# Kernel tuning notes

Measured on AMD Instinct MI355X. Metric: run time of the kernel, lower is better.

The kernel has to match this reference:

```python
import jax, jax.numpy as jnp
import numpy as np

EPS = 1.1920929e-07  # torch RMSNorm default eps = float32 finfo eps

def rms_norm(x, w):
    return x * jax.lax.rsqrt(jnp.mean(x * x, axis=-1, keepdims=True) + EPS) * w

def setup_inputs() -> dict:
    key = jax.random.key(0)
    ks = jax.random.split(key, 10)
    B, C, H, W = 8, 64, 48, 48
    E = C  # embed_dim = query_dim = key_dim = value_dim
    q = jax.random.normal(ks[0], (B, C, H, W), jnp.float32)
    k = jax.random.normal(ks[1], (B, C, H, W), jnp.float32)
    v = jax.random.normal(ks[2], (B, C, H, W), jnp.float32)
    s = 1.0 / np.sqrt(E)
    conv_w = jax.random.normal(ks[3], (C, C, 3, 3), jnp.float32) * (1.0 / np.sqrt(C * 9))
    nq_w = jnp.ones((E,), jnp.float32)
    nk_w = jnp.ones((E,), jnp.float32)
    wq = jax.random.normal(ks[4], (E, E), jnp.float32) * s
    bq = jax.random.normal(ks[5], (E,), jnp.float32) * 0.01
    wk = jax.random.normal(ks[6], (E, E), jnp.float32) * s
    bk = jax.random.normal(ks[7], (E,), jnp.float32) * 0.01
    return {"q": q, "k": k, "v": v, "conv_w": conv_w, "nq_w": nq_w,
            "nk_w": nk_w, "wq": wq, "bq": bq, "wk": wk, "bk": bk}

def reference(q, k, v, conv_w, nq_w, nk_w, wq, bq, wk, bk):
    B, C, H, W = q.shape
    num_heads = 4
    head_dim = C // num_heads
    # conv2d 3x3, stride 1, same padding, no bias
    qc = jax.lax.conv_general_dilated(
        q, conv_w, window_strides=(1, 1), padding='SAME',
        dimension_numbers=('NCHW', 'OIHW', 'NCHW'))
    # b c h w -> b (h w) c
    qs = qc.reshape(B, C, H * W).transpose(0, 2, 1)
    ksq = k.reshape(B, C, -1).transpose(0, 2, 1)
    vsq = v.reshape(B, C, -1).transpose(0, 2, 1)
    # RMSNorm on q and k (norm_v output feeds MHA value path whose output is discarded)
    qn = rms_norm(qs, nq_w)
    kn = rms_norm(ksq, nk_w)
    # MHA projections (q scaled by 1/sqrt(head_dim) as in torch)
    qp = (qn @ wq.T + bq) * (1.0 / np.sqrt(head_dim))
    kp = ksq_p = kn @ wk.T + bk
    Sq, Sk = qp.shape[1], kp.shape[1]
    qh = qp.reshape(B, Sq, num_heads, head_dim)
    kh = kp.reshape(B, Sk, num_heads, head_dim)
    scores = jnp.einsum('bihd,bjhd->bhij', qh, kh)
    attn = jax.nn.softmax(scores, axis=-1)
    # average_attn_weights=True -> mean over heads
    attn_avg = jnp.mean(attn, axis=1)  # [b, i, j]
    # custom output: weighted sum over RAW (un-normed, unprojected) value
    out = jnp.einsum('bij,bjd->bid', attn_avg, vsq)
    return out
```

## Files before the change

kernel.cpp:

```cpp
#include <hip/hip_runtime.h>
#include <hip/hip_bf16.h>

namespace {
constexpr int kB = 8;
constexpr int kC = 64;
constexpr int kH = 48;
constexpr int kW = 48;
constexpr int kS = kH * kW;
constexpr float kEps = 1.1920929e-07f;
constexpr float kQScale = 0.25f * 1.4426950408889634f;
}

typedef __attribute__((ext_vector_type(8))) short short8;
typedef __attribute__((ext_vector_type(4))) float f32x4;

__device__ __forceinline__ short f2bf(float x) {
  unsigned u = __float_as_uint(x);
  u += 0x7fffu + ((u >> 16) & 1u);
  return (short)(u >> 16);
}
__device__ __forceinline__ float bf2f(short s) {
  return __uint_as_float(((unsigned)(unsigned short)s) << 16);
}
__device__ __forceinline__ float fexp2(float x) {
  return __builtin_amdgcn_exp2f(x);
}

__global__ __launch_bounds__(256) void prep_lite(
    const float* __restrict__ v, const float* __restrict__ wq,
    const float* __restrict__ wk, const float* __restrict__ conv_w,
    short* __restrict__ vq, short* __restrict__ wqb3, short* __restrict__ wkb3,
    short* __restrict__ wt3, float* __restrict__ out) {
  const int blk = blockIdx.x;
  const int t = threadIdx.x;
  if (blk < 576) {
    int g = blk * 256 + t;
    int bb = g / 18432;
    int rem = g - bb * 18432;
    int jseg = rem >> 8;
    int sub = rem & 255;
    int d = sub >> 6;
    int Lq = sub & 63;
    const float* src = v + ((size_t)(bb * 64 + d * 16 + (Lq & 15))) * kS
                         + jseg * 32 + (Lq >> 4) * 8;
    float4 x0 = *reinterpret_cast<const float4*>(src);
    float4 x1 = *reinterpret_cast<const float4*>(src + 4);
    short8 o;
    o[0] = f2bf(x0.x); o[1] = f2bf(x0.y); o[2] = f2bf(x0.z); o[3] = f2bf(x0.w);
    o[4] = f2bf(x1.x); o[5] = f2bf(x1.y); o[6] = f2bf(x1.z); o[7] = f2bf(x1.w);
    *reinterpret_cast<short8*>(vq + (size_t)g * 8) = o;
  } else if (blk < 752) {
    int idx = (blk - 576) * 256 + t;
    if (idx < 4096) {
      int j = idx & 7, Lw = (idx >> 3) & 63, slab = idx >> 9;
      int nt = slab & 3, kh = slab >> 2;
      int e = nt * 16 + (Lw & 15), c = kh * 32 + (Lw >> 4) * 8 + j;
      wqb3[idx] = f2bf(wq[e * 64 + c]);
    } else if (idx < 8192) {
      int i2 = idx - 4096;
      int j = i2 & 7, Lw = (i2 >> 3) & 63, slab = i2 >> 9;
      int nt = slab & 3, kh = slab >> 2;
      int e = nt * 16 + (Lw & 15), c = kh * 32 + (Lw >> 4) * 8 + j;
      wkb3[i2] = f2bf(wk[e * 64 + c]);
    } else {
      int i3 = idx - 8192;
      int j = i3 & 7, Lw = (i3 >> 3) & 63, slab = i3 >> 9;
      int nt = slab & 3, kh = (slab >> 2) & 1, tap = slab >> 3;
      int co = nt * 16 + (Lw & 15), ci = kh * 32 + (Lw >> 4) * 8 + j;
      wt3[i3] = f2bf(conv_w[co * 576 + ci * 9 + tap]);
    }
  } else {
    size_t i = (size_t)(blk - 752) * 256 + t;
    float4 z = make_float4(0.f, 0.f, 0.f, 0.f);
    *reinterpret_cast<float4*>(out + i * 8) = z;
    *reinterpret_cast<float4*>(out + i * 8 + 4) = z;
  }
}

__global__ __launch_bounds__(256) void qk_gemm_t(
    const float* __restrict__ q, const float* __restrict__ k,
    const short* __restrict__ wt3, const short* __restrict__ wqb3,
    const short* __restrict__ wkb3,
    const float* __restrict__ nq_w, const float* __restrict__ nk_w,
    const float* __restrict__ bq, const float* __restrict__ bk,
    short* __restrict__ qp, short* __restrict__ kq) {
  __shared__ __align__(16) short Qs[164][72];
  __shared__ __align__(16) short ln[4][16][80];
  __shared__ float tile[64][65];
  const int blk = blockIdx.x;
  const int t = threadIdx.x;
  const int ws = t >> 6;
  const int L = t & 63;
  const int quad = L >> 4;
  const int l16 = L & 15;
  const int tx = t & 63;
  const int ty = t >> 6;
  const short8 zero8 = {0, 0, 0, 0, 0, 0, 0, 0};

  if (blk < 288) {
    const int b = blk / 36;
    const int S0 = (blk % 36) * 64;
    const int sBase = S0 + ws * 16;
    const int s = sBase + l16;
    const int h = s / kW, w = s % kW;

    const float* qb = q + (size_t)b * kC * kS;
#pragma unroll
    for (int p = 0; p < 3; ++p) {
      int scol = S0 - 49 + p * 64 + tx;
      scol = scol < 0 ? 0 : (scol >= kS ? kS - 1 : scol);
#pragma unroll
      for (int r = 0; r < 16; ++r) {
        int c = r * 4 + ty;
        tile[c][tx] = qb[(size_t)c * kS + scol];
      }
      __syncthreads();
#pragma unroll
      for (int r = 0; r < 16; ++r) {
        int j = r * 4 + ty;
        int srow = p * 64 + j;
        if (srow < 164) Qs[srow][tx] = f2bf(tile[tx][j]);
      }
      __syncthreads();
    }

    const int baseLocal = ws * 16 + l16 + 49;
    f32x4 acc[4] = {{0.f, 0.f, 0.f, 0.f}, {0.f, 0.f, 0.f, 0.f},
                    {0.f, 0.f, 0.f, 0.f}, {0.f, 0.f, 0.f, 0.f}};
#pragma unroll
    for (int tap = 0; tap < 9; ++tap) {
      const int dh = tap / 3 - 1, dw = tap % 3 - 1;
      const bool valid = (unsigned)(h + dh) < (unsigned)kH &&
                         (unsigned)(w + dw) < (unsigned)kW;
      const int local = baseLocal + dh * kW + dw;
#pragma unroll
      for (int kh = 0; kh < 2; ++kh) {
        short8 af = *reinterpret_cast<const short8*>(&Qs[local][kh * 32 + quad * 8]);
        af = valid ? af : zero8;
        const short* wb = wt3 + ((tap * 2 + kh) * 4) * 512 + L * 8;
#pragma unroll
        for (int nt = 0; nt < 4; ++nt) {
          short8 bf = *reinterpret_cast<const short8*>(wb + nt * 512);
          acc[nt] = __builtin_amdgcn_mfma_f32_16x16x32_bf16(af, bf, acc[nt], 0, 0, 0);
        }
      }
    }
    float rstd[4];
#pragma unroll
    for (int reg = 0; reg < 4; ++reg) {
      float pr = acc[0][reg] * acc[0][reg] + acc[1][reg] * acc[1][reg]
               + acc[2][reg] * acc[2][reg] + acc[3][reg] * acc[3][reg];
      pr += __shfl_xor(pr, 1, 64);
      pr += __shfl_xor(pr, 2, 64);
      pr += __shfl_xor(pr, 4, 64);
      pr += __shfl_xor(pr, 8, 64);
      rstd[reg] = rsqrtf(pr * (1.0f / kC) + kEps);
    }
#pragma unroll
    for (int nt = 0; nt < 4; ++nt) {
      float g = nq_w[nt * 16 + l16];
#pragma unroll
      for (int reg = 0; reg < 4; ++reg) {
        ln[ws][quad * 4 + reg][nt * 16 + l16] = f2bf(acc[nt][reg] * rstd[reg] * g);
      }
    }
    __syncthreads();
    f32x4 acc2[4] = {{0.f, 0.f, 0.f, 0.f}, {0.f, 0.f, 0.f, 0.f},
                     {0.f, 0.f, 0.f, 0.f}, {0.f, 0.f, 0.f, 0.f}};
#pragma unroll
    for (int kh = 0; kh < 2; ++kh) {
      short8 af = *reinterpret_cast<const short8*>(&ln[ws][l16][kh * 32 + quad * 8]);
      const short* wb = wqb3 + (kh * 4) * 512 + L * 8;
#pragma unroll
      for (int nt = 0; nt < 4; ++nt) {
        short8 bf = *reinterpret_cast<const short8*>(wb + nt * 512);
        acc2[nt] = __builtin_amdgcn_mfma_f32_16x16x32_bf16(af, bf, acc2[nt], 0, 0, 0);
      }
    }
#pragma unroll
    for (int nt = 0; nt < 4; ++nt) {
      const int e = nt * 16 + l16;
      float bias = bq[e];
#pragma unroll
      for (int reg = 0; reg < 4; ++reg) {
        qp[((size_t)b * kS + sBase + quad * 4 + reg) * kC + e] =
            f2bf((acc2[nt][reg] + bias) * kQScale);
      }
    }
  } else {
    const int idx = blk - 288;
    const int b = idx / 36;
    const int S0 = (idx % 36) * 64;
    const int sBase = S0 + ws * 16;

    const float* kb = k + (size_t)b * kC * kS;
#pragma unroll
    for (int r = 0; r < 16; ++r) {
      int c = r * 4 + ty;
      tile[c][tx] = kb[(size_t)c * kS + S0 + tx];
    }
    __syncthreads();
#pragma unroll
    for (int r = 0; r < 16; ++r) {
      int j = r * 4 + ty;
      Qs[j][tx] = f2bf(tile[tx][j]);
    }
    __syncthreads();

    short8 af0 = *reinterpret_cast<const short8*>(&Qs[ws * 16 + l16][quad * 8]);
    short8 af1 = *reinterpret_cast<const short8*>(&Qs[ws * 16 + l16][32 + quad * 8]);

    float xs[16];
#pragma unroll
    for (int j = 0; j < 8; ++j) { xs[j] = bf2f(af0[j]); xs[8 + j] = bf2f(af1[j]); }
    float sum = 0.f;
#pragma unroll
    for (int j = 0; j < 16; ++j) sum = fmaf(xs[j], xs[j], sum);
    sum += __shfl_xor(sum, 16, 64);
    sum += __shfl_xor(sum, 32, 64);
    float rstd = rsqrtf(sum * (1.0f / kC) + kEps);

    const float* n0 = nk_w + quad * 8;
#pragma unroll
    for (int j = 0; j < 8; ++j) {
      af0[j] = f2bf(xs[j] * rstd * n0[j]);
      af1[j] = f2bf(xs[8 + j] * rstd * n0[32 + j]);
    }

    f32x4 acc[4] = {{0.f, 0.f, 0.f, 0.f}, {0.f, 0.f, 0.f, 0.f},
                    {0.f, 0.f, 0.f, 0.f}, {0.f, 0.f, 0.f, 0.f}};
#pragma unroll
    for (int nt = 0; nt < 4; ++nt) {
      short8 bf0 = *reinterpret_cast<const short8*>(
          wkb3 + (0 * 4 + nt) * 512 + L * 8);
      short8 bf1 = *reinterpret_cast<const short8*>(
          wkb3 + (1 * 4 + nt) * 512 + L * 8);
      acc[nt] = __builtin_amdgcn_mfma_f32_16x16x32_bf16(af0, bf0, acc[nt], 0, 0, 0);
      acc[nt] = __builtin_amdgcn_mfma_f32_16x16x32_bf16(af1, bf1, acc[nt], 0, 0, 0);
    }
    short* kqb = kq + (size_t)b * 147456;
#pragma unroll
    for (int nt = 0; nt < 4; ++nt) {
      const int hp = nt >> 1;
      const int quadp = ((nt & 1) << 1) | (l16 >> 3);
      const int elem = l16 & 7;
      float bias = bk[nt * 16 + l16];
#pragma unroll
      for (int reg = 0; reg < 4; ++reg) {
        int s = sBase + quad * 4 + reg;
        int jseg = s >> 5, jrow = s & 31;
        int c = (jrow >> 2) & 1;
        int l16p = ((jrow >> 3) << 2) | (jrow & 3);
        kqb[((((size_t)jseg * 2 + hp) * 2 + c) * 64 + quadp * 16 + l16p) * 8 + elem] =
            f2bf(acc[nt][reg] + bias);
      }
    }
  }
}

#define LOADT(K0, K1, V0, V1, V2, V3, JT)                                      \
  do {                                                                         \
    const short* kb_ = kbase + (size_t)(JT) * 4096;                            \
    const short* vb_ = vbase + (size_t)(JT) * 4096;                            \
    K0 = *reinterpret_cast<const short8*>(kb_);                                \
    K1 = *reinterpret_cast<const short8*>(kb_ + 512);                          \
    V0 = *reinterpret_cast<const short8*>(vb_);                                \
    V1 = *reinterpret_cast<const short8*>(vb_ + 512);                          \
    V2 = *reinterpret_cast<const short8*>(vb_ + 1024);                         \
    V3 = *reinterpret_cast<const short8*>(vb_ + 1536);                         \
  } while (0)

#define PHASE(K0, K1, V0, V1, V2, V3)                                          \
  do {                                                                         \
    _Pragma("unroll")                                                          \
    for (int hl = 0; hl < 2; ++hl) {                                           \
      f32x4 s0 = __builtin_amdgcn_mfma_f32_16x16x32_bf16(K0, qm[hl], zc, 0, 0, 0); \
      f32x4 s1 = __builtin_amdgcn_mfma_f32_16x16x32_bf16(K1, qm[hl], zc, 0, 0, 0); \
      float e0 = fexp2(s0[0]), e1 = fexp2(s0[1]);                              \
      float e2 = fexp2(s0[2]), e3 = fexp2(s0[3]);                              \
      float f0 = fexp2(s1[0]), f1 = fexp2(s1[1]);                              \
      float f2 = fexp2(s1[2]), f3 = fexp2(s1[3]);                              \
      union { __hip_bfloat162 h2[4]; short8 s8; } cv;                          \
      cv.h2[0] = __float22bfloat162_rn(make_float2(e0, e1));                   \
      cv.h2[1] = __float22bfloat162_rn(make_float2(e2, e3));                   \
      cv.h2[2] = __float22bfloat162_rn(make_float2(f0, f1));                   \
      cv.h2[3] = __float22bfloat162_rn(make_float2(f2, f3));                   \
      U[hl][0] = __builtin_amdgcn_mfma_f32_16x16x32_bf16(V0, cv.s8, U[hl][0], 0, 0, 0); \
      U[hl][1] = __builtin_amdgcn_mfma_f32_16x16x32_bf16(V1, cv.s8, U[hl][1], 0, 0, 0); \
      U[hl][2] = __builtin_amdgcn_mfma_f32_16x16x32_bf16(V2, cv.s8, U[hl][2], 0, 0, 0); \
      U[hl][3] = __builtin_amdgcn_mfma_f32_16x16x32_bf16(V3, cv.s8, U[hl][3], 0, 0, 0); \
      Ul[hl]   = __builtin_amdgcn_mfma_f32_16x16x32_bf16(af_l, cv.s8, Ul[hl], 0, 0, 0); \
    }                                                                          \
  } while (0)

__global__ __launch_bounds__(256, 4) void attn_flash(
    const short* __restrict__ qp, const short* __restrict__ kq,
    const short* __restrict__ vq, float* __restrict__ out) {
  __shared__ float pl[4][16][2];
  __shared__ float Li[32][2];
  __shared__ __align__(16) float slab[16][66];

  const int blk = blockIdx.x;
  const int b = blk & 7;
  const int idx = blk >> 3;
  const int hp = idx & 1;
  const int i0 = (idx >> 1) * 32;
  const int t = threadIdx.x;
  const int ws = t >> 6;
  const int isub = ws & 1;
  const int jhalf = ws >> 1;
  const int L = t & 63;
  const int quad = L >> 4;
  const int l16 = L & 15;

  const f32x4 zc = {0.f, 0.f, 0.f, 0.f};
  const short8 z8 = {0, 0, 0, 0, 0, 0, 0, 0};
  const short ob = (short)0x3F80;
  const short8 ones8 = {ob, ob, ob, ob, ob, ob, ob, ob};
  const short8 af_l = (l16 == 0) ? ones8 : z8;

  const short* qrow = qp + ((size_t)b * kS + i0 + isub * 16 + l16) * kC + hp * 32;
  const short8 qw = *reinterpret_cast<const short8*>(qrow + quad * 8);
  const bool lo = quad < 2;
  const short8 qm[2] = {lo ? qw : z8, lo ? z8 : qw};

  const short* kbase =
      kq + (((size_t)(b * 72 + jhalf) * 2 + hp) * 2 * 64 + L) * 8;
  const short* vbase = vq + ((size_t)(b * 72 + jhalf) * 4 * 64 + L) * 8;

  f32x4 U[2][4];
#pragma unroll
  for (int hl = 0; hl < 2; ++hl)
#pragma unroll
    for (int d = 0; d < 4; ++d) U[hl][d] = zc;
  f32x4 Ul[2] = {zc, zc};

  short8 ka0, ka1, va0, va1, va2, va3;
  short8 kb0, kb1, vb0, vb1, vb2, vb3;
  LOADT(ka0, ka1, va0, va1, va2, va3, 0);
  LOADT(kb0, kb1, vb0, vb1, vb2, vb3, 1);

  for (int jt = 0; jt < 34; jt += 2) {
    PHASE(ka0, ka1, va0, va1, va2, va3);
    LOADT(ka0, ka1, va0, va1, va2, va3, jt + 2);
    PHASE(kb0, kb1, vb0, vb1, vb2, vb3);
    LOADT(kb0, kb1, vb0, vb1, vb2, vb3, jt + 3);
  }
  PHASE(ka0, ka1, va0, va1, va2, va3);
  PHASE(kb0, kb1, vb0, vb1, vb2, vb3);

  if (quad == 0) {
#pragma unroll
    for (int hl = 0; hl < 2; ++hl) pl[ws][l16][hl] = Ul[hl][0];
  }
  __syncthreads();
  if (t < 64) {
    const int i = t >> 1, h2 = t & 1;
    Li[i][h2] = 0.25f / (pl[i >> 4][i & 15][h2] + pl[(i >> 4) + 2][i & 15][h2]);
  }
  __syncthreads();
  float c2[2];
#pragma unroll
  for (int hl = 0; hl < 2; ++hl) c2[hl] = Li[isub * 16 + l16][hl];

#pragma unroll
  for (int d = 0; d < 4; ++d) {
    if (jhalf == 1) {
#pragma unroll
      for (int hl = 0; hl < 2; ++hl)
#pragma unroll
        for (int reg = 0; reg < 4; ++reg)
          slab[(isub * 2 + hl) * 4 + reg][L] = U[hl][d][reg];
    }
    __syncthreads();
    if (jhalf == 0) {
      float of[4] = {0.f, 0.f, 0.f, 0.f};
#pragma unroll
      for (int hl = 0; hl < 2; ++hl) {
#pragma unroll
        for (int reg = 0; reg < 4; ++reg) {
          float tot = U[hl][d][reg] + slab[(isub * 2 + hl) * 4 + reg][L];
          of[reg] += tot * c2[hl];
        }
      }
      float* op = out + ((size_t)b * kS + i0 + isub * 16 + l16) * kC + d * 16 + quad * 4;
#pragma unroll
      for (int reg = 0; reg < 4; ++reg) atomicAdd(op + reg, of[reg]);
    }
    __syncthreads();
  }
}

extern "C" void kernel_launch(void* const* d_in, const int* in_sizes, int n_in,
                              void* d_out, int out_size, void* d_ws, size_t ws_size,
                              hipStream_t stream) {
  const float* q      = (const float*)d_in[0];
  const float* k      = (const float*)d_in[1];
  const float* v      = (const float*)d_in[2];
  const float* conv_w = (const float*)d_in[3];
  const float* nq_w   = (const float*)d_in[4];
  const float* nk_w   = (const float*)d_in[5];
  const float* wq     = (const float*)d_in[6];
  const float* bq     = (const float*)d_in[7];
  const float* wk     = (const float*)d_in[8];
  const float* bk     = (const float*)d_in[9];
  float* out = (float*)d_out;

  const size_t N = (size_t)kB * kS * kC;
  short* vq   = (short*)d_ws;
  short* qp   = vq + N;
  short* kq   = qp + N;
  short* wqb3 = kq + N;
  short* wkb3 = wqb3 + 4096;
  short* wt3  = wkb3 + 4096;

  prep_lite<<<1328, 256, 0, stream>>>(v, wq, wk, conv_w,
                                      vq, wqb3, wkb3, wt3, out);
  qk_gemm_t<<<576, 256, 0, stream>>>(q, k, wt3, wqb3, wkb3,
                                     nq_w, nk_w, bq, bk, qp, kq);
  attn_flash<<<1152, 256, 0, stream>>>(qp, kq, vq, out);
}
```

Baseline: 144.0 us.

## Split attention key range four ways per block with 16-row query tiles

The flash attention kernel now gives each block 16 query rows instead of 32. Its four waves each walk a quarter of the key sequence, rather than two waves per query subtile each walking half. The launch doubles to 2304 blocks and occupancy bounds rise to 8 blocks per CU, to expose more parallelism and shorten each wave's serial loop. In exchange, each K/V tile loaded serves only one 16-row query tile, so K/V traffic through cache doubles. The LDS cross-wave reduction also now combines four partials.

Result: slower. 368.2 us (+155.7%).

```diff
diff --git a/kernel.cpp b/kernel.cpp
--- a/kernel.cpp
+++ b/kernel.cpp
@@ -258,10 +258,10 @@
   }
 }
 
-#define LOADT(K0, K1, V0, V1, V2, V3, JT)                                      \
+#define LOADT(K0, K1, V0, V1, V2, V3, IT)                                      \
   do {                                                                         \
-    const short* kb_ = kbase + (size_t)(JT) * 4096;                            \
-    const short* vb_ = vbase + (size_t)(JT) * 4096;                            \
+    const short* kb_ = kbase + (size_t)(IT) * 8192;                            \
+    const short* vb_ = vbase + (size_t)(IT) * 8192;                            \
     K0 = *reinterpret_cast<const short8*>(kb_);                                \
     K1 = *reinterpret_cast<const short8*>(kb_ + 512);                          \
     V0 = *reinterpret_cast<const short8*>(vb_);                                \
@@ -293,22 +293,20 @@
     }                                                                          \
   } while (0)
 
-__global__ __launch_bounds__(256, 4) void attn_flash(
+__global__ __launch_bounds__(256, 8) void attn_flash(
     const short* __restrict__ qp, const short* __restrict__ kq,
     const short* __restrict__ vq, float* __restrict__ out) {
   __shared__ float pl[4][16][2];
-  __shared__ float Li[32][2];
-  __shared__ __align__(16) float slab[16][66];
+  __shared__ float Li[16][2];
+  __shared__ __align__(16) float slab[3][8][66];
 
   const int blk = blockIdx.x;
   const int b = blk & 7;
   const int idx = blk >> 3;
   const int hp = idx & 1;
-  const int i0 = (idx >> 1) * 32;
+  const int i0 = (idx >> 1) * 16;
   const int t = threadIdx.x;
   const int ws = t >> 6;
-  const int isub = ws & 1;
-  const int jhalf = ws >> 1;
   const int L = t & 63;
   const int quad = L >> 4;
   const int l16 = L & 15;
@@ -319,14 +317,14 @@
   const short8 ones8 = {ob, ob, ob, ob, ob, ob, ob, ob};
   const short8 af_l = (l16 == 0) ? ones8 : z8;
 
-  const short* qrow = qp + ((size_t)b * kS + i0 + isub * 16 + l16) * kC + hp * 32;
+  const short* qrow = qp + ((size_t)b * kS + i0 + l16) * kC + hp * 32;
   const short8 qw = *reinterpret_cast<const short8*>(qrow + quad * 8);
   const bool lo = quad < 2;
   const short8 qm[2] = {lo ? qw : z8, lo ? z8 : qw};
 
   const short* kbase =
-      kq + (((size_t)(b * 72 + jhalf) * 2 + hp) * 2 * 64 + L) * 8;
-  const short* vbase = vq + ((size_t)(b * 72 + jhalf) * 4 * 64 + L) * 8;
+      kq + ((((size_t)(b * 72 + ws) * 2 + hp) * 2) * 64 + L) * 8;
+  const short* vbase = vq + (((size_t)(b * 72 + ws) * 4) * 64 + L) * 8;
 
   f32x4 U[2][4];
 #pragma unroll
@@ -340,11 +338,11 @@
   LOADT(ka0, ka1, va0, va1, va2, va3, 0);
   LOADT(kb0, kb1, vb0, vb1, vb2, vb3, 1);
 
-  for (int jt = 0; jt < 34; jt += 2) {
+  for (int it = 0; it < 16; it += 2) {
     PHASE(ka0, ka1, va0, va1, va2, va3);
-    LOADT(ka0, ka1, va0, va1, va2, va3, jt + 2);
+    LOADT(ka0, ka1, va0, va1, va2, va3, it + 2);
     PHASE(kb0, kb1, vb0, vb1, vb2, vb3);
-    LOADT(kb0, kb1, vb0, vb1, vb2, vb3, jt + 3);
+    LOADT(kb0, kb1, vb0, vb1, vb2, vb3, it + 3);
   }
   PHASE(ka0, ka1, va0, va1, va2, va3);
   PHASE(kb0, kb1, vb0, vb1, vb2, vb3);
@@ -354,36 +352,37 @@
     for (int hl = 0; hl < 2; ++hl) pl[ws][l16][hl] = Ul[hl][0];
   }
   __syncthreads();
-  if (t < 64) {
+  if (t < 32) {
     const int i = t >> 1, h2 = t & 1;
-    Li[i][h2] = 0.25f / (pl[i >> 4][i & 15][h2] + pl[(i >> 4) + 2][i & 15][h2]);
+    Li[i][h2] = 0.25f / (pl[0][i][h2] + pl[1][i][h2] + pl[2][i][h2] + pl[3][i][h2]);
   }
   __syncthreads();
   float c2[2];
 #pragma unroll
-  for (int hl = 0; hl < 2; ++hl) c2[hl] = Li[isub * 16 + l16][hl];
+  for (int hl = 0; hl < 2; ++hl) c2[hl] = Li[l16][hl];
 
 #pragma unroll
   for (int d = 0; d < 4; ++d) {
-    if (jhalf == 1) {
+    if (ws != 0) {
 #pragma unroll
       for (int hl = 0; hl < 2; ++hl)
 #pragma unroll
         for (int reg = 0; reg < 4; ++reg)
-          slab[(isub * 2 + hl) * 4 + reg][L] = U[hl][d][reg];
+          slab[ws - 1][hl * 4 + reg][L] = U[hl][d][reg];
     }
     __syncthreads();
-    if (jhalf == 0) {
+    if (ws == 0) {
       float of[4] = {0.f, 0.f, 0.f, 0.f};
 #pragma unroll
       for (int hl = 0; hl < 2; ++hl) {
 #pragma unroll
         for (int reg = 0; reg < 4; ++reg) {
-          float tot = U[hl][d][reg] + slab[(isub * 2 + hl) * 4 + reg][L];
+          float tot = U[hl][d][reg] + slab[0][hl * 4 + reg][L]
+                    + slab[1][hl * 4 + reg][L] + slab[2][hl * 4 + reg][L];
           of[reg] += tot * c2[hl];
         }
       }
-      float* op = out + ((size_t)b * kS + i0 + isub * 16 + l16) * kC + d * 16 + quad * 4;
+      float* op = out + ((size_t)b * kS + i0 + l16) * kC + d * 16 + quad * 4;
 #pragma unroll
       for (int reg = 0; reg < 4; ++reg) atomicAdd(op + reg, of[reg]);
     }
@@ -418,5 +417,5 @@
                                       vq, wqb3, wkb3, wt3, out);
   qk_gemm_t<<<576, 256, 0, stream>>>(q, k, wt3, wqb3, wkb3,
                                      nq_w, nk_w, bq, bk, qp, kq);
-  attn_flash<<<1152, 256, 0, stream>>>(qp, kq, vq, out);
-}
+  attn_flash<<<2304, 256, 0, stream>>>(qp, kq, vq, out);
+}
```
